# Optimization experiments

Measured on AMD Instinct MI355X. Metric: run time of the kernel, lower is better.

The kernel has to match this reference:

```python
import jax, jax.numpy as jnp
import numpy as np


def setup_inputs() -> dict:
    key = jax.random.key(0)
    x = jax.random.normal(key, (16, 3, 1024, 1024), dtype=jnp.float32)
    return {"x": x, "win_size": 3}


def reference(x, win_size):
    # DCP: pad spatially, extract KxK sliding windows (stride 1), min over
    # channel dim, then L1 norm (sum of abs) over everything.
    # min over channels commutes with window extraction, so take the
    # channel-min of the padded image first, then do a KxK sliding-window
    # sum of |min| via a ones-kernel convolution (avoids the huge
    # [B,H,W,K,K] unfold tensor while computing identical math).
    K = win_size
    p = K // 2
    xp = jnp.pad(x, ((0, 0), (0, 0), (p, p), (p, p)))          # [B,C,Hp,Wp]
    m = jnp.abs(jnp.min(xp, axis=1, keepdims=True))             # [B,1,Hp,Wp]
    ones = jnp.ones((1, 1, K, K), dtype=x.dtype)
    win_sums = jax.lax.conv_general_dilated(
        m, ones, window_strides=(1, 1), padding="VALID",
        dimension_numbers=("NCHW", "OIHW", "NCHW"))             # [B,1,H,W]
    return jnp.sum(win_sums)
```

## Files before the change

kernel.cpp:

```cpp
#include <hip/hip_runtime.h>


#define DCP_HW (1024 * 1024)
#define GROUPS_PER_IMG (DCP_HW / 4)
#define NGROUPS (16 * GROUPS_PER_IMG)

#define NBLOCKS 2048
#define NTHREADS 256
#define NTOTAL (NBLOCKS * NTHREADS)
#define ITERS (NGROUPS / NTOTAL)

__global__ __launch_bounds__(NTHREADS) void dcp_partial_kernel(
    const float* __restrict__ x, double* __restrict__ part) {
  const unsigned t = blockIdx.x * NTHREADS + threadIdx.x;

  const unsigned rem = (t & (GROUPS_PER_IMG - 1)) << 2;
  const unsigned h = rem >> 10;
  const unsigned wcol = rem & 1023;
  const unsigned b0 = t >> 18;
  const float wx0 = (wcol == 0) ? 2.0f : 3.0f;
  const float wx3 = (wcol == 1020) ? 2.0f : 3.0f;
  const float wy = (h == 0 || h == 1023) ? 2.0f : 3.0f;

  const float* p = x + (size_t)(b0 * 3) * DCP_HW + rem;

  float s0 = 0.0f, smid = 0.0f, s3 = 0.0f;

  #pragma unroll
  for (int half = 0; half < 2; ++half) {
    float4 a[4][3];
    #pragma unroll
    for (int i = 0; i < 4; ++i) {
      const float* q = p + (size_t)(half * 4 + i) * (6 * DCP_HW);
      a[i][0] = *reinterpret_cast<const float4*>(q);
      a[i][1] = *reinterpret_cast<const float4*>(q + DCP_HW);
      a[i][2] = *reinterpret_cast<const float4*>(q + 2 * DCP_HW);
    }
    #pragma unroll
    for (int i = 0; i < 4; ++i) {
      s0   += fabsf(fminf(fminf(a[i][0].x, a[i][1].x), a[i][2].x));
      smid += fabsf(fminf(fminf(a[i][0].y, a[i][1].y), a[i][2].y))
            + fabsf(fminf(fminf(a[i][0].z, a[i][1].z), a[i][2].z));
      s3   += fabsf(fminf(fminf(a[i][0].w, a[i][1].w), a[i][2].w));
    }
  }
  const float accf = wy * (s0 * wx0 + smid * 3.0f + s3 * wx3);

  double d = (double)accf;
  #pragma unroll
  for (int off = 32; off > 0; off >>= 1) d += __shfl_down(d, off, 64);

  __shared__ double lds[NTHREADS / 64];
  const int lane = threadIdx.x & 63;
  const int wv = threadIdx.x >> 6;
  if (lane == 0) lds[wv] = d;
  __syncthreads();
  if (threadIdx.x == 0) {
    part[blockIdx.x] = lds[0] + lds[1] + lds[2] + lds[3];
  }
}

__global__ __launch_bounds__(256) void dcp_final_kernel(
    const double* __restrict__ part, float* __restrict__ out, int npart) {
  double d = 0.0;
  for (int i = threadIdx.x; i < npart; i += 256) d += part[i];
  #pragma unroll
  for (int off = 32; off > 0; off >>= 1) d += __shfl_down(d, off, 64);

  __shared__ double lds[4];
  const int lane = threadIdx.x & 63;
  const int wv = threadIdx.x >> 6;
  if (lane == 0) lds[wv] = d;
  __syncthreads();
  if (threadIdx.x == 0) out[0] = (float)(lds[0] + lds[1] + lds[2] + lds[3]);
}

extern "C" void kernel_launch(void* const* d_in, const int* in_sizes, int n_in,
                              void* d_out, int out_size, void* d_ws, size_t ws_size,
                              hipStream_t stream) {
  const float* x = (const float*)d_in[0];
  float* out = (float*)d_out;
  double* part = (double*)d_ws;

  dcp_partial_kernel<<<NBLOCKS, NTHREADS, 0, stream>>>(x, part);
  dcp_final_kernel<<<1, 256, 0, stream>>>(part, out, NBLOCKS);
}
```

Before: 274.4 us.

## Map one wavefront per image row and simplify edge weighting

Result: no change. 272.7 us (-0.6%).

```diff
diff --git a/kernel.cpp b/kernel.cpp
--- a/kernel.cpp
+++ b/kernel.cpp
@@ -2,57 +2,52 @@
 
 
 #define DCP_HW (1024 * 1024)
-#define GROUPS_PER_IMG (DCP_HW / 4)
-#define NGROUPS (16 * GROUPS_PER_IMG)
-
-#define NBLOCKS 2048
+#define NROWS (16 * 1024)
+#define NBLOCKS (NROWS / 4)
 #define NTHREADS 256
-#define NTOTAL (NBLOCKS * NTHREADS)
-#define ITERS (NGROUPS / NTOTAL)
 
 __global__ __launch_bounds__(NTHREADS) void dcp_partial_kernel(
     const float* __restrict__ x, double* __restrict__ part) {
-  const unsigned t = blockIdx.x * NTHREADS + threadIdx.x;
+  const unsigned lane = threadIdx.x & 63;
+  const unsigned wv = threadIdx.x >> 6;
+  const unsigned R = blockIdx.x * 4 + wv;
+  const unsigned b = R >> 10;
+  const unsigned h = R & 1023;
 
-  const unsigned rem = (t & (GROUPS_PER_IMG - 1)) << 2;
-  const unsigned h = rem >> 10;
-  const unsigned wcol = rem & 1023;
-  const unsigned b0 = t >> 18;
-  const float wx0 = (wcol == 0) ? 2.0f : 3.0f;
-  const float wx3 = (wcol == 1020) ? 2.0f : 3.0f;
+  const float* q0 = x + (size_t)b * (3 * DCP_HW) + (size_t)h * 1024 + 4 * lane;
+
+  float4 a[3][4];
+  #pragma unroll
+  for (int ch = 0; ch < 3; ++ch) {
+    const float* q = q0 + ch * DCP_HW;
+    #pragma unroll
+    for (int j = 0; j < 4; ++j)
+      a[ch][j] = *reinterpret_cast<const float4*>(q + 256 * j);
+  }
+
+  float4 m[4];
+  #pragma unroll
+  for (int j = 0; j < 4; ++j) {
+    m[j].x = fabsf(fminf(fminf(a[0][j].x, a[1][j].x), a[2][j].x));
+    m[j].y = fabsf(fminf(fminf(a[0][j].y, a[1][j].y), a[2][j].y));
+    m[j].z = fabsf(fminf(fminf(a[0][j].z, a[1][j].z), a[2][j].z));
+    m[j].w = fabsf(fminf(fminf(a[0][j].w, a[1][j].w), a[2][j].w));
+  }
+
+  float s_all = 0.0f;
+  #pragma unroll
+  for (int j = 0; j < 4; ++j) s_all += (m[j].x + m[j].y) + (m[j].z + m[j].w);
+
+  const float c0 = (lane == 0) ? m[0].x : 0.0f;
+  const float c3 = (lane == 63) ? m[3].w : 0.0f;
   const float wy = (h == 0 || h == 1023) ? 2.0f : 3.0f;
-
-  const float* p = x + (size_t)(b0 * 3) * DCP_HW + rem;
-
-  float s0 = 0.0f, smid = 0.0f, s3 = 0.0f;
-
-  #pragma unroll
-  for (int half = 0; half < 2; ++half) {
-    float4 a[4][3];
-    #pragma unroll
-    for (int i = 0; i < 4; ++i) {
-      const float* q = p + (size_t)(half * 4 + i) * (6 * DCP_HW);
-      a[i][0] = *reinterpret_cast<const float4*>(q);
-      a[i][1] = *reinterpret_cast<const float4*>(q + DCP_HW);
-      a[i][2] = *reinterpret_cast<const float4*>(q + 2 * DCP_HW);
-    }
-    #pragma unroll
-    for (int i = 0; i < 4; ++i) {
-      s0   += fabsf(fminf(fminf(a[i][0].x, a[i][1].x), a[i][2].x));
-      smid += fabsf(fminf(fminf(a[i][0].y, a[i][1].y), a[i][2].y))
-            + fabsf(fminf(fminf(a[i][0].z, a[i][1].z), a[i][2].z));
-      s3   += fabsf(fminf(fminf(a[i][0].w, a[i][1].w), a[i][2].w));
-    }
-  }
-  const float accf = wy * (s0 * wx0 + smid * 3.0f + s3 * wx3);
+  const float accf = wy * (3.0f * s_all - c0 - c3);
 
   double d = (double)accf;
   #pragma unroll
   for (int off = 32; off > 0; off >>= 1) d += __shfl_down(d, off, 64);
 
   __shared__ double lds[NTHREADS / 64];
-  const int lane = threadIdx.x & 63;
-  const int wv = threadIdx.x >> 6;
   if (lane == 0) lds[wv] = d;
   __syncthreads();
   if (threadIdx.x == 0) {
```
